# Kernel tuning notes

Hardware: AMD Instinct MI355X
Metric: run time of the kernel (lower is better)

The kernel has to match this reference:

```python
import jax, jax.numpy as jnp
import numpy as np

N = 100000
E = 1600000
IN, HID, OUT = 128, 64, 32


def setup_inputs() -> dict:
    key = jax.random.key(0)
    ks = jax.random.split(key, 8)
    x = jax.random.normal(ks[0], (N, IN), dtype=jnp.float32)
    edge_index = jax.random.randint(ks[1], (2, E), 0, N, dtype=jnp.int32)
    eps = jax.random.normal(ks[2], (N, OUT), dtype=jnp.float32)
    W1 = jax.random.normal(ks[3], (IN, HID), dtype=jnp.float32) / np.sqrt(IN)
    b1 = jnp.zeros((HID,), jnp.float32)
    Wmu = jax.random.normal(ks[4], (HID, OUT), dtype=jnp.float32) / np.sqrt(HID)
    bmu = jnp.zeros((OUT,), jnp.float32)
    Wls = jax.random.normal(ks[5], (HID, OUT), dtype=jnp.float32) / np.sqrt(HID)
    bls = jnp.zeros((OUT,), jnp.float32)
    return dict(x=x, edge_index=edge_index, eps=eps, W1=W1, b1=b1,
                Wmu=Wmu, bmu=bmu, Wls=Wls, bls=bls)


def reference(x, edge_index, eps, W1, b1, Wmu, bmu, Wls, bls):
    n = x.shape[0]
    src, dst = edge_index[0], edge_index[1]
    # GCN with self-loops and symmetric normalization (PyG GCNConv default)
    loop = jnp.arange(n, dtype=src.dtype)
    s = jnp.concatenate([src, loop])   # [E+N]
    d = jnp.concatenate([dst, loop])
    deg = jax.ops.segment_sum(jnp.ones_like(s, jnp.float32), d, num_segments=n)
    dis = jax.lax.rsqrt(jnp.maximum(deg, 1.0))  # deg >= 1 due to self-loops
    norm = dis[s] * dis[d]                       # [E+N]

    def gcn_conv(h, W, b):
        h = h @ W                                # transform first (small dim)
        msg = h[s] * norm[:, None]               # gather over edges
        return jax.ops.segment_sum(msg, d, num_segments=n) + b

    h = jax.nn.relu(gcn_conv(x, W1, b1))
    # F.normalize(h, p=2, dim=-1)
    h = h / jnp.maximum(jnp.linalg.norm(h, axis=-1, keepdims=True), 1e-12)
    mu = gcn_conv(h, Wmu, bmu)
    logstd = gcn_conv(h, Wls, bls)
    # reparametrize (training mode): mu + randn * exp(clamp(logstd, -10, 10))
    z = mu + eps * jnp.exp(jnp.clip(logstd, -10.0, 10.0))
    # decode: sigmoid(<z_i, z_j>) over original edges
    adj_pred = jax.nn.sigmoid(jnp.sum(z[src] * z[dst], axis=1))
    return adj_pred, mu, logstd
```

## Files before the change

### kernel.cpp

```cpp
#include <hip/hip_runtime.h>
#include <hip/hip_fp16.h>

#define NN 100000
#define NE 1600000
#define W_BKT 128
#define NB_BKT ((NN + W_BKT - 1) / W_BKT)
#define TILE_E 16384
#define NT ((NE + TILE_E - 1) / TILE_E)
#define STAGE_CAP 4352

typedef _Float16 half2v __attribute__((ext_vector_type(2)));
typedef _Float16 half4v __attribute__((ext_vector_type(4)));
typedef _Float16 half8v __attribute__((ext_vector_type(8)));
typedef float float2v __attribute__((ext_vector_type(2)));
typedef float float4v __attribute__((ext_vector_type(4)));


__global__ __launch_bounds__(256) void k_cnt(const int* __restrict__ dst,
                                             int* __restrict__ counts) {
    __shared__ int hc[NB_BKT];
    int tid = threadIdx.x;
    for (int i = tid; i < NB_BKT; i += 256) hc[i] = 0;
    __syncthreads();
    int base = blockIdx.x * TILE_E;
    int lim = base + TILE_E; if (lim > NE) lim = NE;
    for (int e = base + tid; e < lim; e += 256)
        atomicAdd(&hc[dst[e] >> 7], 1);
    __syncthreads();
    for (int i = tid; i < NB_BKT; i += 256)
        counts[blockIdx.x * NB_BKT + i] = hc[i];
}

__global__ __launch_bounds__(1024) void k_bscan(const int* __restrict__ counts,
                                                int* __restrict__ bucket_base) {
    __shared__ int buf[1024];
    int tid = threadIdx.x;
    int total = 0;
    if (tid < NB_BKT)
        for (int t = 0; t < NT; ++t) total += counts[t * NB_BKT + tid];
    buf[tid] = total;
    __syncthreads();
    for (int off = 1; off < 1024; off <<= 1) {
        int v = (tid >= off) ? buf[tid - off] : 0;
        __syncthreads();
        buf[tid] += v;
        __syncthreads();
    }
    if (tid < NB_BKT) bucket_base[tid] = buf[tid] - total;
    if (tid == 0) bucket_base[NB_BKT] = NE;
}

__global__ __launch_bounds__(256) void k_offs(const int* __restrict__ bucket_base,
                                              int* __restrict__ counts) {
    int b = blockIdx.x * 256 + threadIdx.x;
    if (b >= NB_BKT) return;
    int off = bucket_base[b];
    for (int t = 0; t < NT; ++t) {
        int c = counts[t * NB_BKT + b];
        counts[t * NB_BKT + b] = off;
        off += c;
    }
}

__global__ __launch_bounds__(256) void k_place(const int* __restrict__ src,
                                               const int* __restrict__ dst,
                                               const int* __restrict__ counts,
                                               int* __restrict__ ebuf) {
    __shared__ int cur[NB_BKT];
    int tid = threadIdx.x;
    for (int i = tid; i < NB_BKT; i += 256)
        cur[i] = counts[blockIdx.x * NB_BKT + i];
    __syncthreads();
    int base = blockIdx.x * TILE_E;
    int lim = base + TILE_E; if (lim > NE) lim = NE;
    for (int e = base + tid; e < lim; e += 256) {
        int s = src[e], d = dst[e];
        int pos = atomicAdd(&cur[d >> 7], 1);
        ebuf[pos] = (s << 7) | (d & 127);
    }
}

__global__ __launch_bounds__(256) void k_build(const int* __restrict__ bucket_base,
                                               const int* __restrict__ ebuf,
                                               int* __restrict__ csr_src,
                                               int* __restrict__ row_ptr,
                                               float* __restrict__ dis) {
    __shared__ int deg[W_BKT];
    __shared__ int pre[W_BKT];
    __shared__ int cur[W_BKT];
    __shared__ int stage[STAGE_CAP];
    int b = blockIdx.x;
    int tid = threadIdx.x;
    int beg = bucket_base[b], end = bucket_base[b + 1];
    int n = end - beg;
    if (tid < W_BKT) deg[tid] = 0;
    __syncthreads();
    bool fits = (n <= STAGE_CAP);
    if (fits) {
        for (int i = tid; i < n; i += 256) {
            int val = ebuf[beg + i];
            stage[i] = val;
            atomicAdd(&deg[val & 127], 1);
        }
    } else {
        for (int i = tid; i < n; i += 256)
            atomicAdd(&deg[ebuf[beg + i] & 127], 1);
    }
    __syncthreads();
    if (tid < W_BKT) pre[tid] = deg[tid];
    __syncthreads();
    for (int off = 1; off < W_BKT; off <<= 1) {
        int v = (tid >= off && tid < W_BKT) ? pre[tid - off] : 0;
        __syncthreads();
        if (tid < W_BKT) pre[tid] += v;
        __syncthreads();
    }
    if (tid < W_BKT) {
        int v = b * W_BKT + tid;
        int rp = beg + pre[tid] - deg[tid];
        if (v < NN) {
            row_ptr[v] = rp;
            dis[v] = rsqrtf((float)(1 + deg[tid]));
        }
        cur[tid] = rp;
    }
    if (b == NB_BKT - 1 && tid == 0) row_ptr[NN] = NE;
    __syncthreads();
    if (fits) {
        for (int i = tid; i < n; i += 256) {
            int val = stage[i];
            int pos = atomicAdd(&cur[val & 127], 1);
            csr_src[pos] = val >> 7;
        }
    } else {
        for (int i = tid; i < n; i += 256) {
            int val = ebuf[beg + i];
            int pos = atomicAdd(&cur[val & 127], 1);
            csr_src[pos] = val >> 7;
        }
    }
}


__global__ __launch_bounds__(256) void k_wprep(const float* __restrict__ W1,
                                               const float* __restrict__ Wmu,
                                               const float* __restrict__ Wls,
                                               _Float16* __restrict__ wf1h,
                                               _Float16* __restrict__ wf1l,
                                               _Float16* __restrict__ wf2h,
                                               _Float16* __restrict__ wf2l) {
    int tid = threadIdx.x;
    for (int f = tid; f < 4 * 4 * 64; f += 256) {
        int lane = f & 63;
        int kc = (f >> 6) & 3;
        int ct = f >> 8;
        int col = ct * 16 + (lane & 15);
        int k0 = kc * 32 + (lane >> 4) * 8;
#pragma unroll
        for (int j = 0; j < 8; ++j) {
            float w = W1[(k0 + j) * 64 + col];
            _Float16 hi = (_Float16)w;
            wf1h[f * 8 + j] = hi;
            wf1l[f * 8 + j] = (_Float16)(w - (float)hi);
        }
    }
    for (int f = tid; f < 4 * 2 * 64; f += 256) {
        int lane = f & 63;
        int kc = (f >> 6) & 1;
        int ct = f >> 7;
        int col = ct * 16 + (lane & 15);
        int k0 = kc * 32 + (lane >> 4) * 8;
#pragma unroll
        for (int j = 0; j < 8; ++j) {
            int k = k0 + j;
            float w = (col < 32) ? Wmu[k * 32 + col] : Wls[k * 32 + (col - 32)];
            _Float16 hi = (_Float16)w;
            wf2h[f * 8 + j] = hi;
            wf2l[f * 8 + j] = (_Float16)(w - (float)hi);
        }
    }
}

__device__ __forceinline__ void split8(const float4 a, const float4 b,
                                       half8v& hi, half8v& lo) {
    float v[8] = {a.x, a.y, a.z, a.w, b.x, b.y, b.z, b.w};
#pragma unroll
    for (int i = 0; i < 8; ++i) {
        _Float16 h = (_Float16)v[i];
        hi[i] = h;
        lo[i] = (_Float16)(v[i] - (float)h);
    }
}

__global__ __launch_bounds__(256) void k_gemm1(const float* __restrict__ x,
                                               const _Float16* __restrict__ wf1h,
                                               const _Float16* __restrict__ wf1l,
                                               const float* __restrict__ dis,
                                               _Float16* __restrict__ t1) {
    int tid = threadIdx.x;
    int lane = tid & 63;
    int wv = tid >> 6;
    int wrow = blockIdx.x * 64 + wv * 16;
    int cl = lane & 15, kg = lane >> 4;
    const half8v* Bh = (const half8v*)wf1h;
    const half8v* Bl = (const half8v*)wf1l;
    float4v acc[4] = {};
    int r = wrow + cl;
    long rr = (r < NN) ? r : (NN - 1);
    const float4* xp = (const float4*)(x + rr * 128);
#pragma unroll
    for (int kc = 0; kc < 4; ++kc) {
        float4 xa = xp[kc * 8 + kg * 2];
        float4 xb = xp[kc * 8 + kg * 2 + 1];
        half8v ah, al;
        split8(xa, xb, ah, al);
#pragma unroll
        for (int ct = 0; ct < 4; ++ct) {
            half8v bh = Bh[(ct * 4 + kc) * 64 + lane];
            half8v bl = Bl[(ct * 4 + kc) * 64 + lane];
            acc[ct] = __builtin_amdgcn_mfma_f32_16x16x32_f16(ah, bh, acc[ct], 0, 0, 0);
            acc[ct] = __builtin_amdgcn_mfma_f32_16x16x32_f16(al, bh, acc[ct], 0, 0, 0);
            acc[ct] = __builtin_amdgcn_mfma_f32_16x16x32_f16(ah, bl, acc[ct], 0, 0, 0);
        }
    }
#pragma unroll
    for (int j = 0; j < 4; ++j) {
        int row = wrow + kg * 4 + j;
        if (row < NN) {
            float dv = dis[row];
#pragma unroll
            for (int ct = 0; ct < 4; ++ct)
                t1[(long)row * 64 + ct * 16 + cl] = (_Float16)(acc[ct][j] * dv);
        }
    }
}

__global__ __launch_bounds__(256) void k_gemm2(const float* __restrict__ h,
                                               const _Float16* __restrict__ wf2h,
                                               const _Float16* __restrict__ wf2l,
                                               const float* __restrict__ dis,
                                               _Float16* __restrict__ t2) {
    int tid = threadIdx.x;
    int lane = tid & 63;
    int wv = tid >> 6;
    int wrow = blockIdx.x * 64 + wv * 16;
    int cl = lane & 15, kg = lane >> 4;
    const half8v* Bh = (const half8v*)wf2h;
    const half8v* Bl = (const half8v*)wf2l;
    float4v acc[4] = {};
    int r = wrow + cl;
    long rr = (r < NN) ? r : (NN - 1);
    const float4* hp = (const float4*)(h + rr * 64);
#pragma unroll
    for (int kc = 0; kc < 2; ++kc) {
        float4 xa = hp[kc * 8 + kg * 2];
        float4 xb = hp[kc * 8 + kg * 2 + 1];
        half8v ah, al;
        split8(xa, xb, ah, al);
#pragma unroll
        for (int ct = 0; ct < 4; ++ct) {
            half8v bh = Bh[(ct * 2 + kc) * 64 + lane];
            half8v bl = Bl[(ct * 2 + kc) * 64 + lane];
            acc[ct] = __builtin_amdgcn_mfma_f32_16x16x32_f16(ah, bh, acc[ct], 0, 0, 0);
            acc[ct] = __builtin_amdgcn_mfma_f32_16x16x32_f16(al, bh, acc[ct], 0, 0, 0);
            acc[ct] = __builtin_amdgcn_mfma_f32_16x16x32_f16(ah, bl, acc[ct], 0, 0, 0);
        }
    }
#pragma unroll
    for (int j = 0; j < 4; ++j) {
        int row = wrow + kg * 4 + j;
        if (row < NN) {
            float dv = dis[row];
#pragma unroll
            for (int ct = 0; ct < 4; ++ct)
                t2[(long)row * 64 + ct * 16 + cl] = (_Float16)(acc[ct][j] * dv);
        }
    }
}


#define SWZ_LD(K) r[K] = t4[(__builtin_amdgcn_ds_swizzle(idx, ((K) << 5) | 0x10) << 4) + j4];

__device__ __forceinline__ void batch16_full(const half4v* __restrict__ t4, int idx,
                                             int j4, float* a) {
    half4v r[16];
    SWZ_LD(0)  SWZ_LD(1)  SWZ_LD(2)  SWZ_LD(3)
    SWZ_LD(4)  SWZ_LD(5)  SWZ_LD(6)  SWZ_LD(7)
    SWZ_LD(8)  SWZ_LD(9)  SWZ_LD(10) SWZ_LD(11)
    SWZ_LD(12) SWZ_LD(13) SWZ_LD(14) SWZ_LD(15)
#pragma unroll
    for (int k = 0; k < 16; ++k) {
        a[0] += (float)r[k][0]; a[1] += (float)r[k][1];
        a[2] += (float)r[k][2]; a[3] += (float)r[k][3];
    }
}

__device__ __forceinline__ void batch16_mask(const half4v* __restrict__ t4, int idx,
                                             int j4, int cnt, float* a) {
    half4v r[16];
    SWZ_LD(0)  SWZ_LD(1)  SWZ_LD(2)  SWZ_LD(3)
    SWZ_LD(4)  SWZ_LD(5)  SWZ_LD(6)  SWZ_LD(7)
    SWZ_LD(8)  SWZ_LD(9)  SWZ_LD(10) SWZ_LD(11)
    SWZ_LD(12) SWZ_LD(13) SWZ_LD(14) SWZ_LD(15)
#pragma unroll
    for (int k = 0; k < 16; ++k) {
        float w = (k < cnt) ? 1.0f : 0.0f;
        a[0] += w * (float)r[k][0]; a[1] += w * (float)r[k][1];
        a[2] += w * (float)r[k][2]; a[3] += w * (float)r[k][3];
    }
}

__device__ __forceinline__ void batch8_mask(const half4v* __restrict__ t4, int idx,
                                            int j4, int cnt, float* a) {
    half4v r[8];
    SWZ_LD(0)  SWZ_LD(1)  SWZ_LD(2)  SWZ_LD(3)
    SWZ_LD(4)  SWZ_LD(5)  SWZ_LD(6)  SWZ_LD(7)
#pragma unroll
    for (int k = 0; k < 8; ++k) {
        float w = (k < cnt) ? 1.0f : 0.0f;
        a[0] += w * (float)r[k][0]; a[1] += w * (float)r[k][1];
        a[2] += w * (float)r[k][2]; a[3] += w * (float)r[k][3];
    }
}

__global__ __launch_bounds__(256) void k_agg1(const half4v* __restrict__ tv4,
                                              const int* __restrict__ row_ptr,
                                              const int* __restrict__ csr_src,
                                              const float* __restrict__ dis,
                                              const float* __restrict__ b1,
                                              float* __restrict__ h) {
    int lane = threadIdx.x & 63;
    int j4 = lane & 15;
    int v = blockIdx.x * 16 + (threadIdx.x >> 6) * 4 + (lane >> 4);
    int beg = row_ptr[v], end = row_ptr[v + 1];
    float a[4] = {0.f, 0.f, 0.f, 0.f};
    int base = beg;
    for (; base + 16 <= end; base += 16) {
        int idx = csr_src[base + j4];
        batch16_full(tv4, idx, j4, a);
    }
    int cnt = end - base;
    if (cnt > 0) {
        int idx = csr_src[base + ((j4 < cnt) ? j4 : cnt - 1)];
        if (cnt > 8) batch16_mask(tv4, idx, j4, cnt, a);
        else         batch8_mask(tv4, idx, j4, cnt, a);
    }
    float dv = dis[v];
    half4v rv = tv4[(v << 4) + j4];
    float4 bb = ((const float4*)b1)[j4];
    float val0 = fmaxf(dv * (a[0] + (float)rv[0]) + bb.x, 0.0f);
    float val1 = fmaxf(dv * (a[1] + (float)rv[1]) + bb.y, 0.0f);
    float val2 = fmaxf(dv * (a[2] + (float)rv[2]) + bb.z, 0.0f);
    float val3 = fmaxf(dv * (a[3] + (float)rv[3]) + bb.w, 0.0f);
    float ss = val0 * val0 + val1 * val1 + val2 * val2 + val3 * val3;
#pragma unroll
    for (int m = 1; m < 16; m <<= 1) ss += __shfl_xor(ss, m);
    float scale = 1.0f / fmaxf(sqrtf(ss), 1e-12f);
    float4v* h4 = (float4v*)h;
    float4v hv; hv.x = val0 * scale; hv.y = val1 * scale;
    hv.z = val2 * scale; hv.w = val3 * scale;
    h4[(v << 4) + j4] = hv;
}

__global__ __launch_bounds__(256) void k_agg2(const half4v* __restrict__ tv4,
                                              const int* __restrict__ row_ptr,
                                              const int* __restrict__ csr_src,
                                              const float* __restrict__ dis,
                                              const float* __restrict__ bmu,
                                              const float* __restrict__ bls,
                                              const float* __restrict__ eps,
                                              float* __restrict__ mu,
                                              float* __restrict__ ls,
                                              _Float16* __restrict__ zh) {
    int lane = threadIdx.x & 63;
    int j4 = lane & 15;
    int v = blockIdx.x * 16 + (threadIdx.x >> 6) * 4 + (lane >> 4);
    int beg = row_ptr[v], end = row_ptr[v + 1];
    float a[4] = {0.f, 0.f, 0.f, 0.f};
    int base = beg;
    for (; base + 16 <= end; base += 16) {
        int idx = csr_src[base + j4];
        batch16_full(tv4, idx, j4, a);
    }
    int cnt = end - base;
    if (cnt > 0) {
        int idx = csr_src[base + ((j4 < cnt) ? j4 : cnt - 1)];
        if (cnt > 8) batch16_mask(tv4, idx, j4, cnt, a);
        else         batch8_mask(tv4, idx, j4, cnt, a);
    }
    float dv = dis[v];
    half4v rv = tv4[(v << 4) + j4];
    float4 bb = (j4 < 8) ? ((const float4*)bmu)[j4] : ((const float4*)bls)[j4 - 8];
    float val0 = dv * (a[0] + (float)rv[0]) + bb.x;
    float val1 = dv * (a[1] + (float)rv[1]) + bb.y;
    float val2 = dv * (a[2] + (float)rv[2]) + bb.z;
    float val3 = dv * (a[3] + (float)rv[3]) + bb.w;
    float o0 = __shfl_xor(val0, 8);
    float o1 = __shfl_xor(val1, 8);
    float o2 = __shfl_xor(val2, 8);
    float o3 = __shfl_xor(val3, 8);
    float4v* mu4 = (float4v*)mu;
    float4v* ls4 = (float4v*)ls;
    half4v* z4  = (half4v*)zh;
    const float4* e4 = (const float4*)eps;
    if (j4 < 8) {
        float4v mv; mv.x = val0; mv.y = val1; mv.z = val2; mv.w = val3;
        __builtin_nontemporal_store(mv, &mu4[(v << 3) + j4]);
        float4 ev = e4[(v << 3) + j4];
        float l0 = fminf(fmaxf(o0, -10.0f), 10.0f);
        float l1 = fminf(fmaxf(o1, -10.0f), 10.0f);
        float l2 = fminf(fmaxf(o2, -10.0f), 10.0f);
        float l3 = fminf(fmaxf(o3, -10.0f), 10.0f);
        half4v zw;
        zw[0] = (_Float16)(val0 + ev.x * expf(l0));
        zw[1] = (_Float16)(val1 + ev.y * expf(l1));
        zw[2] = (_Float16)(val2 + ev.z * expf(l2));
        zw[3] = (_Float16)(val3 + ev.w * expf(l3));
        z4[(v << 3) + j4] = zw;
    } else {
        float4v lv; lv.x = val0; lv.y = val1; lv.z = val2; lv.w = val3;
        __builtin_nontemporal_store(lv, &ls4[(v << 3) + (j4 - 8)]);
    }
}

__global__ __launch_bounds__(256) void k_decode(const _Float16* __restrict__ zh,
                                                const int* __restrict__ src,
                                                const int* __restrict__ dst,
                                                float* __restrict__ out) {
    long t = (long)blockIdx.x * 256 + threadIdx.x;
    long e = t >> 2; int l = (int)(t & 3);
    if (e >= NE) return;
    int s = src[e], d = dst[e];
    const half8v* z8 = (const half8v*)zh;
    half8v a = z8[s * 4 + l];
    half8v b = z8[d * 4 + l];
    float p = 0.f;
#pragma unroll
    for (int i = 0; i < 8; ++i) p += (float)a[i] * (float)b[i];
    p += __shfl_xor(p, 1);
    p += __shfl_xor(p, 2);
    if (l == 0) out[e] = 1.0f / (1.0f + expf(-p));
}

extern "C" void kernel_launch(void* const* d_in, const int* in_sizes, int n_in,
                              void* d_out, int out_size, void* d_ws, size_t ws_size,
                              hipStream_t stream) {
    const float* x   = (const float*)d_in[0];
    const int*   ei  = (const int*)d_in[1];
    const float* eps = (const float*)d_in[2];
    const float* W1  = (const float*)d_in[3];
    const float* b1  = (const float*)d_in[4];
    const float* Wmu = (const float*)d_in[5];
    const float* bmu = (const float*)d_in[6];
    const float* Wls = (const float*)d_in[7];
    const float* bls = (const float*)d_in[8];
    const int* src = ei;
    const int* dst = ei + NE;

    float* out = (float*)d_out;
    float* adj = out;
    float* mu  = out + NE;
    float* ls  = mu + (long)NN * 32;

    float* dis      = (float*)d_ws;
    int*   row_ptr  = (int*)(dis + NN);
    int*   bucket_base = row_ptr + 100004;
    int*   counts   = bucket_base + 784;
    int*   ebuf     = counts + 76640;
    int*   csr_src  = ebuf + NE;
    _Float16* t     = (_Float16*)(csr_src + NE);
    float* h        = (float*)(t + (long)NN * 64);
    _Float16* zh    = (_Float16*)(h + (long)NN * 64 + 12);

    _Float16* wf1h = (_Float16*)counts;
    _Float16* wf1l = wf1h + 8192;
    _Float16* wf2h = wf1l + 8192;
    _Float16* wf2l = wf2h + 4096;

    const int B = 256;

    k_cnt  <<<NT, B, 0, stream>>>(dst, counts);
    k_bscan<<<1, 1024, 0, stream>>>(counts, bucket_base);
    k_offs <<<(NB_BKT + B - 1) / B, B, 0, stream>>>(bucket_base, counts);
    k_place<<<NT, B, 0, stream>>>(src, dst, counts, ebuf);
    k_wprep<<<1, B, 0, stream>>>(W1, Wmu, Wls, wf1h, wf1l, wf2h, wf2l);
    k_build<<<NB_BKT, B, 0, stream>>>(bucket_base, ebuf, csr_src, row_ptr, dis);

    k_gemm1<<<(NN + 63) / 64, B, 0, stream>>>(x, wf1h, wf1l, dis, t);
    k_agg1 <<<NN / 16, B, 0, stream>>>((const half4v*)t, row_ptr, csr_src, dis, b1, h);

    k_gemm2<<<(NN + 63) / 64, B, 0, stream>>>(h, wf2h, wf2l, dis, t);
    k_agg2 <<<NN / 16, B, 0, stream>>>((const half4v*)t, row_ptr, csr_src, dis,
                                       bmu, bls, eps, mu, ls, zh);

    k_decode<<<(int)(((long)NE * 4 + B - 1) / B), B, 0, stream>>>(zh, src, dst, adj);
}
```

Measured before the change: 348.4 us.

## Store normalized hidden in fp16, fold offset pass into scan, enlarge agg blocks

```diff
diff --git a/kernel.cpp b/kernel.cpp
--- a/kernel.cpp
+++ b/kernel.cpp
@@ -31,7 +31,7 @@
         counts[blockIdx.x * NB_BKT + i] = hc[i];
 }
 
-__global__ __launch_bounds__(1024) void k_bscan(const int* __restrict__ counts,
+__global__ __launch_bounds__(1024) void k_bscan(int* __restrict__ counts,
                                                 int* __restrict__ bucket_base) {
     __shared__ int buf[1024];
     int tid = threadIdx.x;
@@ -46,20 +46,16 @@
         buf[tid] += v;
         __syncthreads();
     }
-    if (tid < NB_BKT) bucket_base[tid] = buf[tid] - total;
+    if (tid < NB_BKT) {
+        int off = buf[tid] - total;
+        bucket_base[tid] = off;
+        for (int t = 0; t < NT; ++t) {
+            int c = counts[t * NB_BKT + tid];
+            counts[t * NB_BKT + tid] = off;
+            off += c;
+        }
+    }
     if (tid == 0) bucket_base[NB_BKT] = NE;
-}
-
-__global__ __launch_bounds__(256) void k_offs(const int* __restrict__ bucket_base,
-                                              int* __restrict__ counts) {
-    int b = blockIdx.x * 256 + threadIdx.x;
-    if (b >= NB_BKT) return;
-    int off = bucket_base[b];
-    for (int t = 0; t < NT; ++t) {
-        int c = counts[t * NB_BKT + b];
-        counts[t * NB_BKT + b] = off;
-        off += c;
-    }
 }
 
 __global__ __launch_bounds__(256) void k_place(const int* __restrict__ src,
@@ -235,7 +231,7 @@
     }
 }
 
-__global__ __launch_bounds__(256) void k_gemm2(const float* __restrict__ h,
+__global__ __launch_bounds__(256) void k_gemm2(const _Float16* __restrict__ h,
                                                const _Float16* __restrict__ wf2h,
                                                const _Float16* __restrict__ wf2l,
                                                const float* __restrict__ dis,
@@ -250,19 +246,15 @@
     float4v acc[4] = {};
     int r = wrow + cl;
     long rr = (r < NN) ? r : (NN - 1);
-    const float4* hp = (const float4*)(h + rr * 64);
+    const half8v* hp = (const half8v*)(h + rr * 64);
 #pragma unroll
     for (int kc = 0; kc < 2; ++kc) {
-        float4 xa = hp[kc * 8 + kg * 2];
-        float4 xb = hp[kc * 8 + kg * 2 + 1];
-        half8v ah, al;
-        split8(xa, xb, ah, al);
+        half8v ah = hp[kc * 4 + kg];
 #pragma unroll
         for (int ct = 0; ct < 4; ++ct) {
             half8v bh = Bh[(ct * 2 + kc) * 64 + lane];
             half8v bl = Bl[(ct * 2 + kc) * 64 + lane];
             acc[ct] = __builtin_amdgcn_mfma_f32_16x16x32_f16(ah, bh, acc[ct], 0, 0, 0);
-            acc[ct] = __builtin_amdgcn_mfma_f32_16x16x32_f16(al, bh, acc[ct], 0, 0, 0);
             acc[ct] = __builtin_amdgcn_mfma_f32_16x16x32_f16(ah, bl, acc[ct], 0, 0, 0);
         }
     }
@@ -323,15 +315,15 @@
     }
 }
 
-__global__ __launch_bounds__(256) void k_agg1(const half4v* __restrict__ tv4,
+__global__ __launch_bounds__(512) void k_agg1(const half4v* __restrict__ tv4,
                                               const int* __restrict__ row_ptr,
                                               const int* __restrict__ csr_src,
                                               const float* __restrict__ dis,
                                               const float* __restrict__ b1,
-                                              float* __restrict__ h) {
+                                              _Float16* __restrict__ h) {
     int lane = threadIdx.x & 63;
     int j4 = lane & 15;
-    int v = blockIdx.x * 16 + (threadIdx.x >> 6) * 4 + (lane >> 4);
+    int v = blockIdx.x * 32 + (threadIdx.x >> 6) * 4 + (lane >> 4);
     int beg = row_ptr[v], end = row_ptr[v + 1];
     float a[4] = {0.f, 0.f, 0.f, 0.f};
     int base = beg;
@@ -356,13 +348,14 @@
 #pragma unroll
     for (int m = 1; m < 16; m <<= 1) ss += __shfl_xor(ss, m);
     float scale = 1.0f / fmaxf(sqrtf(ss), 1e-12f);
-    float4v* h4 = (float4v*)h;
-    float4v hv; hv.x = val0 * scale; hv.y = val1 * scale;
-    hv.z = val2 * scale; hv.w = val3 * scale;
+    half4v* h4 = (half4v*)h;
+    half4v hv;
+    hv[0] = (_Float16)(val0 * scale); hv[1] = (_Float16)(val1 * scale);
+    hv[2] = (_Float16)(val2 * scale); hv[3] = (_Float16)(val3 * scale);
     h4[(v << 4) + j4] = hv;
 }
 
-__global__ __launch_bounds__(256) void k_agg2(const half4v* __restrict__ tv4,
+__global__ __launch_bounds__(512) void k_agg2(const half4v* __restrict__ tv4,
                                               const int* __restrict__ row_ptr,
                                               const int* __restrict__ csr_src,
                                               const float* __restrict__ dis,
@@ -374,7 +367,7 @@
                                               _Float16* __restrict__ zh) {
     int lane = threadIdx.x & 63;
     int j4 = lane & 15;
-    int v = blockIdx.x * 16 + (threadIdx.x >> 6) * 4 + (lane >> 4);
+    int v = blockIdx.x * 32 + (threadIdx.x >> 6) * 4 + (lane >> 4);
     int beg = row_ptr[v], end = row_ptr[v + 1];
     float a[4] = {0.f, 0.f, 0.f, 0.f};
     int base = beg;
@@ -469,8 +462,8 @@
     int*   ebuf     = counts + 76640;
     int*   csr_src  = ebuf + NE;
     _Float16* t     = (_Float16*)(csr_src + NE);
-    float* h        = (float*)(t + (long)NN * 64);
-    _Float16* zh    = (_Float16*)(h + (long)NN * 64 + 12);
+    _Float16* h     = t + (long)NN * 64;
+    _Float16* zh    = h + (long)NN * 64 + 24;
 
     _Float16* wf1h = (_Float16*)counts;
     _Float16* wf1l = wf1h + 8192;
@@ -481,17 +474,16 @@
 
     k_cnt  <<<NT, B, 0, stream>>>(dst, counts);
     k_bscan<<<1, 1024, 0, stream>>>(counts, bucket_base);
-    k_offs <<<(NB_BKT + B - 1) / B, B, 0, stream>>>(bucket_base, counts);
     k_place<<<NT, B, 0, stream>>>(src, dst, counts, ebuf);
     k_wprep<<<1, B, 0, stream>>>(W1, Wmu, Wls, wf1h, wf1l, wf2h, wf2l);
     k_build<<<NB_BKT, B, 0, stream>>>(bucket_base, ebuf, csr_src, row_ptr, dis);
 
     k_gemm1<<<(NN + 63) / 64, B, 0, stream>>>(x, wf1h, wf1l, dis, t);
-    k_agg1 <<<NN / 16, B, 0, stream>>>((const half4v*)t, row_ptr, csr_src, dis, b1, h);
+    k_agg1 <<<NN / 32, 512, 0, stream>>>((const half4v*)t, row_ptr, csr_src, dis, b1, h);
 
     k_gemm2<<<(NN + 63) / 64, B, 0, stream>>>(h, wf2h, wf2l, dis, t);
-    k_agg2 <<<NN / 16, B, 0, stream>>>((const half4v*)t, row_ptr, csr_src, dis,
-                                       bmu, bls, eps, mu, ls, zh);
+    k_agg2 <<<NN / 32, 512, 0, stream>>>((const half4v*)t, row_ptr, csr_src, dis,
+                                         bmu, bls, eps, mu, ls, zh);
 
     k_decode<<<(int)(((long)NE * 4 + B - 1) / B), B, 0, stream>>>(zh, src, dst, adj);
 }
```

Result: slower. 359.2 us (+3.1%).
